# Kernel optimization log

Hardware: AMD Instinct MI355X
Metric: run time of the kernel (lower is better)

## Reference

```python
import jax, jax.numpy as jnp
import numpy as np

LMAX = 4
DSH = (LMAX + 1) ** 2          # 25 spherical-harmonic coefficients
C = 32                          # channels per degree l
N = 10000                       # nodes
E = 160000                      # edges
FC = 64                         # fc_len_in (radial/edge scalar feature dim)

# flattened (l,m) index = l^2 + l + m
IDX0 = np.array([l * l + l for l in range(LMAX + 1)])               # m = 0 coeffs
POS = {m: np.array([l * l + l + m for l in range(m, LMAX + 1)]) for m in range(1, LMAX + 1)}
NEG = {m: np.array([l * l + l - m for l in range(m, LMAX + 1)]) for m in range(1, LMAX + 1)}
L_OF_IDX = np.concatenate([np.full(2 * l + 1, l) for l in range(LMAX + 1)])  # degree of each coeff


def setup_inputs() -> dict:
    key = jax.random.key(0)
    ks = jax.random.split(key, 20)
    inp = {
        "x": jax.random.normal(ks[0], (N, DSH, C), jnp.float32),
        "wigner": jax.random.normal(ks[1], (E, DSH, DSH), jnp.float32) * 0.2,
        "edge_fc": jax.random.normal(ks[2], (E, FC), jnp.float32),
        "edge_src": jax.random.randint(ks[3], (E,), 0, N),
        "edge_dst": jax.random.randint(ks[4], (E,), 0, N),
    }
    # per-m SO(2) block weights
    d0 = (LMAX + 1) * C
    inp["w0"] = jax.random.normal(ks[5], (d0, d0), jnp.float32) / np.sqrt(d0)
    k = 6
    for m in range(1, LMAX + 1):
        dm = (LMAX + 1 - m) * C
        inp[f"w{m}r"] = jax.random.normal(ks[k], (dm, dm), jnp.float32) / np.sqrt(dm); k += 1
        inp[f"w{m}i"] = jax.random.normal(ks[k], (dm, dm), jnp.float32) / np.sqrt(dm); k += 1
    # radial/cfconv network producing per-(degree, channel) scales
    inp["fc_w"] = jax.random.normal(ks[k], (FC, (LMAX + 1) * C), jnp.float32) / np.sqrt(FC)
    inp["fc_b"] = jnp.zeros(((LMAX + 1) * C,), jnp.float32)
    return inp


def reference(x, wigner, edge_fc, edge_src, edge_dst,
              w0, w1r, w1i, w2r, w2i, w3r, w3i, w4r, w4i, fc_w, fc_b):
    Wr = {1: w1r, 2: w2r, 3: w3r, 4: w4r}
    Wi = {1: w1i, 2: w2i, 3: w3i, 4: w4i}
    # gather node features to edges and rotate into edge-aligned frame
    xe = x[edge_src]                                   # [E, 25, C]
    xr = jnp.einsum('eij,ejc->eic', wigner, xe)        # [E, 25, C]
    Ee = xr.shape[0]
    y = jnp.zeros_like(xr)
    # m = 0 block: real linear over stacked-l channels
    x0 = xr[:, IDX0, :].reshape(Ee, -1)                # [E, 5*C]
    y = y.at[:, IDX0, :].set((x0 @ w0).reshape(Ee, LMAX + 1, C))
    # m > 0 blocks: SO(2) complex-style mixing
    for m in range(1, LMAX + 1):
        pos, neg = POS[m], NEG[m]
        Lm = len(pos)
        xp = xr[:, pos, :].reshape(Ee, -1)             # [E, Lm*C]
        xn = xr[:, neg, :].reshape(Ee, -1)
        yp = xp @ Wr[m] - xn @ Wi[m]
        yn = xp @ Wi[m] + xn @ Wr[m]
        y = y.at[:, pos, :].set(yp.reshape(Ee, Lm, C))
        y = y.at[:, neg, :].set(yn.reshape(Ee, Lm, C))
    # cfconv: per-edge radial scaling, one scalar per (degree, channel)
    scale = jax.nn.silu(edge_fc @ fc_w + fc_b).reshape(Ee, LMAX + 1, C)
    y = y * scale[:, L_OF_IDX, :]
    # rotate back (Wigner D is orthogonal -> transpose is inverse)
    yb = jnp.einsum('eji,ejc->eic', wigner, y)
    # scatter-aggregate messages to destination nodes
    return jax.ops.segment_sum(yb, edge_dst, num_segments=N)
```

## Files before the change

kernel.cpp:

```cpp
#include <hip/hip_runtime.h>

typedef __attribute__((ext_vector_type(8))) short short8;
typedef __attribute__((ext_vector_type(4))) short short4v;
typedef __attribute__((ext_vector_type(4))) float f32x4;

#define MFMA16(a,b,c) __builtin_amdgcn_mfma_f32_16x16x32_bf16((a),(b),(c),0,0,0)

__device__ __align__(16) short g_wt[117760];
__device__ __align__(16) short g_wtf[148480];
__device__ __align__(16) short g_fcwt[10240];

struct K2Tab {
  int   fbase[50];
  int   pboff[50][8];
  short acoeff[50][8];
  short len[50];
  short dm[50];
  short ut[50];
  short ocoeff[50];
  short lsc[50];
  short co16[50];
  short pu[290];
  short pk[290];
};

constexpr K2Tab make_k2tab() {
  K2Tab T{};
  const int P[5][5]  = {{0,2,6,12,20},{3,7,13,21,0},{8,14,22,0,0},{15,23,0,0,0},{24,0,0,0,0}};
  const int Ng[5][5] = {{0,0,0,0,0},{1,5,11,19,0},{4,10,18,0,0},{9,17,0,0,0},{16,0,0,0,0}};
  const int WR[5]  = {0, 25600, 74752, 102400, 114688};
  const int WI[5]  = {0, 41984, 83968, 106496, 115712};
  const int NWI[5] = {0, 58368, 93184, 110592, 116736};
  const int ms[9]  = {1,1,2,2,0,3,3,4,4};
  const int hs[9]  = {0,1,0,1,0,0,1,0,1};
  const int ntc[9] = {8,8,6,6,10,4,4,2,2};
  int u = 0, fb = 0, np = 0;
  for (int g = 0; g < 9; ++g) {
    const int m = ms[g], h = hs[g];
    const int dm = (m == 0) ? 160 : (5 - m) * 32;
    const int lm = (m == 0) ? 5 : (5 - m);
    const int len = (m == 0) ? 5 : 2 * lm;
    const int b1 = (m == 0) ? 0 : ((h == 0) ? WR[m] : WI[m]);
    const int b2 = (m == 0) ? 0 : ((h == 0) ? NWI[m] : WR[m]);
    for (int tt = 0; tt < ntc[g]; ++tt, ++u) {
      T.dm[u] = (short)dm; T.len[u] = (short)len; T.ut[u] = (short)tt;
      const int lo = tt >> 1;
      T.ocoeff[u] = (short)((m == 0) ? P[0][lo] : ((h == 0) ? P[m][lo] : Ng[m][lo]));
      T.lsc[u] = (short)(m + lo);
      T.co16[u] = (short)((tt & 1) * 16);
      T.fbase[u] = fb;
      for (int k = 0; k < len; ++k) {
        int bb, ac;
        if (m == 0)      { bb = k * 32;            ac = P[0][k]; }
        else if (k < lm) { bb = b1 + k * 32;       ac = P[m][k]; }
        else             { bb = b2 + (k - lm) * 32; ac = Ng[m][k - lm]; }
        T.pboff[u][k] = bb; T.acoeff[u][k] = (short)ac;
        T.pu[np] = (short)u; T.pk[np] = (short)k; ++np;
      }
      fb += len * 512;
    }
  }
  return T;
}
__constant__ K2Tab c_kt = make_k2tab();

__device__ __forceinline__ short f2bf(float f) {
  unsigned u = __float_as_uint(f);
  u += 0x7FFFu + ((u >> 16) & 1u);
  return (short)(u >> 16);
}

__global__ void prep_weights(const float* __restrict__ w0,
    const float* __restrict__ w1r, const float* __restrict__ w1i,
    const float* __restrict__ w2r, const float* __restrict__ w2i,
    const float* __restrict__ w3r, const float* __restrict__ w3i,
    const float* __restrict__ w4r, const float* __restrict__ w4i,
    const float* __restrict__ fcw) {
  int idx = blockIdx.x * 256 + threadIdx.x;
  if (idx >= 128000) return;
  if (idx >= 117760) {
    int local = idx - 117760;
    int n = local >> 6, k = local & 63;
    g_fcwt[local] = f2bf(fcw[k * 160 + n]);
    return;
  }
  int off, dm; const float* src; bool neg = false;
  if (idx < 25600)       { off = 0;      dm = 160; src = w0;  }
  else if (idx < 41984)  { off = 25600;  dm = 128; src = w1r; }
  else if (idx < 58368)  { off = 41984;  dm = 128; src = w1i; }
  else if (idx < 74752)  { off = 58368;  dm = 128; src = w1i; neg = true; }
  else if (idx < 83968)  { off = 74752;  dm = 96;  src = w2r; }
  else if (idx < 93184)  { off = 83968;  dm = 96;  src = w2i; }
  else if (idx < 102400) { off = 93184;  dm = 96;  src = w2i; neg = true; }
  else if (idx < 106496) { off = 102400; dm = 64;  src = w3r; }
  else if (idx < 110592) { off = 106496; dm = 64;  src = w3i; }
  else if (idx < 114688) { off = 110592; dm = 64;  src = w3i; neg = true; }
  else if (idx < 115712) { off = 114688; dm = 32;  src = w4r; }
  else if (idx < 116736) { off = 115712; dm = 32;  src = w4i; }
  else                   { off = 116736; dm = 32;  src = w4i; neg = true; }
  int local = idx - off;
  int n = local / dm, k = local - n * dm;
  float v = src[k * dm + n];
  g_wt[idx] = f2bf(neg ? -v : v);
}

__global__ void prep_frags() {
  int i = blockIdx.x * 256 + threadIdx.x;
  if (i >= 290 * 512) return;
  int p = i >> 9;
  int w = i & 511;
  int lane = w >> 3, j = w & 7;
  int l15 = lane & 15, lg = lane >> 4;
  int u = c_kt.pu[p], k = c_kt.pk[p];
  int col = (int)c_kt.ut[u] * 16 + l15;
  g_wtf[i] = g_wt[c_kt.pboff[u][k] + col * (int)c_kt.dm[u] + lg * 8 + j];
}

__global__ void hist_kernel(const int* __restrict__ edst, int* __restrict__ cnt, int E) {
  int i = blockIdx.x * 256 + threadIdx.x;
  if (i < E) atomicAdd(&cnt[edst[i]], 1);
}

__global__ __launch_bounds__(1024) void scan_kernel(
    const int* __restrict__ cnt, int* __restrict__ cursor, int N) {
  __shared__ int s[1024];
  const int t = threadIdx.x;
  int v[10]; int sum = 0;
  #pragma unroll
  for (int k = 0; k < 10; ++k) {
    int i = t * 10 + k;
    v[k] = (i < N) ? cnt[i] : 0;
    sum += v[k];
  }
  s[t] = sum;
  __syncthreads();
  for (int d = 1; d < 1024; d <<= 1) {
    int add = (t >= d) ? s[t - d] : 0;
    __syncthreads();
    s[t] += add;
    __syncthreads();
  }
  int prefix = s[t] - sum;
  #pragma unroll
  for (int k = 0; k < 10; ++k) {
    int i = t * 10 + k;
    if (i < N) cursor[i] = prefix;
    prefix += v[k];
  }
}

__global__ void scatter_kernel(const int* __restrict__ edst, int* __restrict__ cursor,
                               int* __restrict__ order, int E) {
  int i = blockIdx.x * 256 + threadIdx.x;
  if (i < E) {
    int p = atomicAdd(&cursor[edst[i]], 1);
    order[p] = i;
  }
}

#define ESTRIDE 1048
#define SMEM_K12 78080

__global__ __launch_bounds__(512, 4) void k12_fused(
    const float* __restrict__ x, const float* __restrict__ wig,
    const float* __restrict__ efc, const int* __restrict__ esrc,
    const int* __restrict__ order, const float* __restrict__ fcb,
    short* __restrict__ y, int E)
{
  extern __shared__ char smem[];
  short*     s_buf  = (short*)smem;
  _Float16*  s_sc   = (_Float16*)(smem + 67072);
  int*       s_meta = (int*)(smem + 77824);

  const int tid = threadIdx.x;
  const int lane = tid & 63;
  const int wid = tid >> 6;
  const int l15 = lane & 15;
  const int lg  = lane >> 4;
  const int koff = lg * 8;
  const int e0  = blockIdx.x * 32;

  for (int o = tid; o < 3584; o += 512) {
    int e = o / 112, q = o - e * 112;
    ((int*)s_buf)[e * 524 + 400 + q] = 0;
  }
  if (tid < 32) {
    int idx = min(e0 + tid, E - 1);
    int og = order[idx];
    s_meta[tid] = og;
    s_meta[32 + tid] = esrc[og];
  }
  __syncthreads();

  for (int o = tid; o < 25600; o += 512) {
    int e = o / 800, q = o - e * 800;
    s_buf[e * ESTRIDE + q] = f2bf(x[(size_t)s_meta[32 + e] * 800 + q]);
  }
  {
    const int mt = wid >> 2;
    const int ge = s_meta[mt * 16 + l15];
    const float* ep = efc + (size_t)ge * 64;
    float4 fa = *(const float4*)(ep + lg * 8);
    float4 fb = *(const float4*)(ep + lg * 8 + 4);
    float4 fc = *(const float4*)(ep + 32 + lg * 8);
    float4 fd = *(const float4*)(ep + 32 + lg * 8 + 4);
    short8 af0, af1;
    af0[0]=f2bf(fa.x); af0[1]=f2bf(fa.y); af0[2]=f2bf(fa.z); af0[3]=f2bf(fa.w);
    af0[4]=f2bf(fb.x); af0[5]=f2bf(fb.y); af0[6]=f2bf(fb.z); af0[7]=f2bf(fb.w);
    af1[0]=f2bf(fc.x); af1[1]=f2bf(fc.y); af1[2]=f2bf(fc.z); af1[3]=f2bf(fc.w);
    af1[4]=f2bf(fd.x); af1[5]=f2bf(fd.y); af1[6]=f2bf(fd.z); af1[7]=f2bf(fd.w);
    for (int nt = (wid & 3); nt < 10; nt += 4) {
      const int f = nt * 16 + l15;
      const short* bp = g_fcwt + f * 64 + lg * 8;
      short8 b0 = *(const short8*)(bp);
      short8 b1 = *(const short8*)(bp + 32);
      f32x4 acc = {0.f, 0.f, 0.f, 0.f};
      acc = MFMA16(af0, b0, acc);
      acc = MFMA16(af1, b1, acc);
      float bias = fcb[f];
      #pragma unroll
      for (int r = 0; r < 4; ++r) {
        float vv = acc[r] + bias;
        s_sc[(mt * 16 + lg * 4 + r) * 168 + (f >> 5) * 33 + (f & 31)] =
            (_Float16)(vv / (1.f + __expf(-vv)));
      }
    }
  }
  __syncthreads();

  #pragma unroll 4
  for (int i = 0; i < 4; ++i) {
    const int e = wid * 4 + i;
    short* eb = s_buf + e * ESTRIDE;
    const float* wp = wig + (size_t)s_meta[e] * 625;
    short8 a0, a1;
    #pragma unroll
    for (int j = 0; j < 8; ++j) {
      const int k = koff + j;
      a0[j] = eb[k * 32 + l15];
      a1[j] = eb[k * 32 + 16 + l15];
    }
    short8 b0, b1;
    const int r1 = min(16 + l15, 24);
    #pragma unroll
    for (int j = 0; j < 8; ++j) {
      const int k = koff + j;
      const int kc = min(k, 24);
      const short v0 = f2bf(wp[l15 * 25 + kc]);
      const short v1 = f2bf(wp[r1 * 25 + kc]);
      b0[j] = (k < 25) ? v0 : (short)0;
      b1[j] = (k < 25) ? v1 : (short)0;
    }
    f32x4 d00 = {0.f,0.f,0.f,0.f}, d01 = {0.f,0.f,0.f,0.f};
    f32x4 d10 = {0.f,0.f,0.f,0.f}, d11 = {0.f,0.f,0.f,0.f};
    d00 = MFMA16(a0, b0, d00);
    d01 = MFMA16(a0, b1, d01);
    d10 = MFMA16(a1, b0, d10);
    d11 = MFMA16(a1, b1, d11);
    short4v v;
    v[0]=f2bf(d00[0]); v[1]=f2bf(d00[1]); v[2]=f2bf(d00[2]); v[3]=f2bf(d00[3]);
    *(short4v*)(eb + l15 * 32 + lg * 4) = v;
    v[0]=f2bf(d10[0]); v[1]=f2bf(d10[1]); v[2]=f2bf(d10[2]); v[3]=f2bf(d10[3]);
    *(short4v*)(eb + l15 * 32 + 16 + lg * 4) = v;
    if (l15 < 9) {
      v[0]=f2bf(d01[0]); v[1]=f2bf(d01[1]); v[2]=f2bf(d01[2]); v[3]=f2bf(d01[3]);
      *(short4v*)(eb + (16 + l15) * 32 + lg * 4) = v;
      v[0]=f2bf(d11[0]); v[1]=f2bf(d11[1]); v[2]=f2bf(d11[2]); v[3]=f2bf(d11[3]);
      *(short4v*)(eb + (16 + l15) * 32 + 16 + lg * 4) = v;
    }
  }
  __syncthreads();

  for (int u = wid; u < 50; u += 8) {
    const int len = c_kt.len[u];
    const short* Bp = g_wtf + c_kt.fbase[u] + lane * 8;
    short8 B[8];
    #pragma unroll 8
    for (int k = 0; k < 8; ++k)
      if (k < len) B[k] = *(const short8*)(Bp + (k << 9));
    const int co = c_kt.co16[u] + l15;
    const int oc = c_kt.ocoeff[u];
    const int ls = c_kt.lsc[u];
    #pragma unroll 2
    for (int mt = 0; mt < 2; ++mt) {
      const short* xl = s_buf + (mt * 16 + l15) * ESTRIDE + koff;
      f32x4 acc0 = {0.f,0.f,0.f,0.f}, acc1 = {0.f,0.f,0.f,0.f};
      #pragma unroll 8
      for (int k = 0; k < 8; ++k) {
        if (k < len) {
          short8 a = *(const short8*)(xl + (int)c_kt.acoeff[u][k] * 32);
          if (k & 1) acc1 = MFMA16(a, B[k], acc1);
          else       acc0 = MFMA16(a, B[k], acc0);
        }
      }
      f32x4 acc = acc0 + acc1;
      #pragma unroll
      for (int r = 0; r < 4; ++r) {
        const int el = mt * 16 + lg * 4 + r;
        const int slot = e0 + el;
        if (slot < E) {
          float sc = (float)s_sc[el * 168 + ls * 33 + co];
          y[(size_t)slot * 800 + oc * 32 + co] = f2bf(acc[r] * sc);
        }
      }
    }
  }
}

__global__ __launch_bounds__(256, 5) void k3_back(
    const short* __restrict__ y, const float* __restrict__ wig,
    const int* __restrict__ edst, const int* __restrict__ order,
    const int* __restrict__ cnt, float* __restrict__ out, int E)
{
  __shared__ __align__(16) char sumem[27136];
  __shared__ int s_meta[64];
  short* s_y  = (short*)sumem;
  float* yb_s = (float*)sumem;

  const int tid = threadIdx.x;
  const int lane = tid & 63;
  const int wid = tid >> 6;
  const int l15 = lane & 15;
  const int lg  = lane >> 4;
  const int e0  = blockIdx.x * 8;

  for (int o = tid; o < 5216; o += 256) ((int*)sumem)[o] = 0;
  if (tid < 8) {
    int idx = e0 + tid;
    bool v = idx < E;
    int og = order[v ? idx : 0];
    s_meta[tid] = og;
    s_meta[16 + tid] = v ? edst[og] : -1;
  }
  __syncthreads();

  if (wid == 0) {
    int dj = (lane < 8) ? s_meta[16 + lane] : -1;
    bool valid = (lane < 8) && (dj >= 0);
    bool is_start = valid && (lane == 0 || dj != s_meta[16 + lane - 1]);
    unsigned long long vm = __ballot(valid);
    unsigned long long sm = __ballot(is_start);
    int nv = __popcll(vm);
    int ng = __popcll(sm);
    if (lane == 0) s_meta[24] = ng;
    if ((int)lane < ng) {
      int s = -1, c = -1;
      for (int b = 0; b < 8; ++b) { if ((sm >> b) & 1) { ++c; if (c == (int)lane) { s = b; break; } } }
      int e_ = nv;
      for (int b = s + 1; b < 8; ++b) if ((sm >> b) & 1) { e_ = b; break; }
      int d = s_meta[16 + s];
      s_meta[25 + lane] = d;
      s_meta[33 + lane] = s;
      s_meta[41 + lane] = e_;
      s_meta[49 + lane] = ((e_ - s) == cnt[d]) ? 1 : 0;
    }
  }
  for (int o = tid; o < 800; o += 256) {
    int e = o / 100, r = o - e * 100;
    int slot = min(e0 + e, E - 1);
    int q = r * 8;
    *(short8*)(s_y + e * 1304 + (q >> 5) * 40 + (q & 31)) =
        *(const short8*)(y + (size_t)slot * 800 + q);
  }
  __syncthreads();

  f32x4 r00[2], r01[2], r10[2], r11[2];
  #pragma unroll
  for (int i = 0; i < 2; ++i) {
    const int e = wid * 2 + i;
    const short* yb = s_y + e * 1304 + lg * 8 * 40;
    const float* wp = wig + (size_t)s_meta[e] * 625;
    short8 a0, a1, b0, b1;
    const int c2 = min(16 + l15, 24);
    #pragma unroll 8
    for (int j = 0; j < 8; ++j) {
      a0[j] = yb[j * 40 + l15];
      a1[j] = yb[j * 40 + 16 + l15];
      const int k = lg * 8 + j;
      const int kc = min(k, 24);
      const short v0 = f2bf(wp[kc * 25 + l15]);
      const short v1 = f2bf(wp[kc * 25 + c2]);
      b0[j] = (k < 25) ? v0 : (short)0;
      b1[j] = (k < 25) ? v1 : (short)0;
    }
    f32x4 d00 = {0.f,0.f,0.f,0.f}, d01 = {0.f,0.f,0.f,0.f};
    f32x4 d10 = {0.f,0.f,0.f,0.f}, d11 = {0.f,0.f,0.f,0.f};
    d00 = MFMA16(a0, b0, d00);
    d01 = MFMA16(a0, b1, d01);
    d10 = MFMA16(a1, b0, d10);
    d11 = MFMA16(a1, b1, d11);
    r00[i] = d00; r01[i] = d01; r10[i] = d10; r11[i] = d11;
  }
  __syncthreads();

  #pragma unroll
  for (int i = 0; i < 2; ++i) {
    const int e = wid * 2 + i;
    float* yb = yb_s + e * 840;
    #pragma unroll 4
    for (int r = 0; r < 4; ++r) {
      yb[l15 * 33 + lg * 4 + r]      = r00[i][r];
      yb[l15 * 33 + 16 + lg * 4 + r] = r10[i][r];
    }
    if (l15 < 9) {
      #pragma unroll 4
      for (int r = 0; r < 4; ++r) {
        yb[(16 + l15) * 33 + lg * 4 + r]      = r01[i][r];
        yb[(16 + l15) * 33 + 16 + lg * 4 + r] = r11[i][r];
      }
    }
  }
  __syncthreads();

  const int ng = s_meta[24];
  for (int o = tid; o < 800; o += 256) {
    const int yoff = (o >> 5) * 33 + (o & 31);
    for (int g = 0; g < ng; ++g) {
      float sum = 0.f;
      const int gs = s_meta[33 + g], ge = s_meta[41 + g];
      for (int e = gs; e < ge; ++e) sum += yb_s[e * 840 + yoff];
      float* ad = out + (size_t)s_meta[25 + g] * 800 + o;
      if (s_meta[49 + g]) *ad = sum;
      else atomicAdd(ad, sum);
    }
  }
}

extern "C" void kernel_launch(void* const* d_in, const int* in_sizes, int n_in,
                              void* d_out, int out_size, void* d_ws, size_t ws_size,
                              hipStream_t stream) {
  const float* x    = (const float*)d_in[0];
  const float* wigp = (const float*)d_in[1];
  const float* efc  = (const float*)d_in[2];
  const int*   esrc = (const int*)d_in[3];
  const int*   edst = (const int*)d_in[4];
  const float* w0   = (const float*)d_in[5];
  const float* w1r  = (const float*)d_in[6];
  const float* w1i  = (const float*)d_in[7];
  const float* w2r  = (const float*)d_in[8];
  const float* w2i  = (const float*)d_in[9];
  const float* w3r  = (const float*)d_in[10];
  const float* w3i  = (const float*)d_in[11];
  const float* w4r  = (const float*)d_in[12];
  const float* w4i  = (const float*)d_in[13];
  const float* fcw  = (const float*)d_in[14];
  const float* fcb  = (const float*)d_in[15];
  float* out = (float*)d_out;
  const int E = in_sizes[3];
  const int N = out_size / 800;

  int* cnt    = (int*)d_ws;
  int* cursor = cnt + N;
  int* order  = cnt + 2 * N;
  size_t y_off = (((size_t)(2 * N + E) * 4) + 255) & ~(size_t)255;
  short* yb = (short*)((char*)d_ws + y_off);

  hipFuncSetAttribute((const void*)k12_fused,
                      hipFuncAttributeMaxDynamicSharedMemorySize, SMEM_K12);

  prep_weights<<<(128000 + 255) / 256, 256, 0, stream>>>(
      w0, w1r, w1i, w2r, w2i, w3r, w3i, w4r, w4i, fcw);
  prep_frags<<<(290 * 512 + 255) / 256, 256, 0, stream>>>();

  hipMemsetAsync(d_out, 0, (size_t)out_size * sizeof(float), stream);
  hipMemsetAsync(cnt, 0, (size_t)N * sizeof(int), stream);

  hist_kernel<<<(E + 255) / 256, 256, 0, stream>>>(edst, cnt, E);
  scan_kernel<<<1, 1024, 0, stream>>>(cnt, cursor, N);
  scatter_kernel<<<(E + 255) / 256, 256, 0, stream>>>(edst, cursor, order, E);

  k12_fused<<<(E + 31) / 32, 512, SMEM_K12, stream>>>(
      x, wigp, efc, esrc, order, fcb, yb, E);
  k3_back<<<(E + 7) / 8, 256, 0, stream>>>(yb, wigp, edst, order, cnt, out, E);
}
```

Baseline: 770.3 us.

## Fuse forward rotation, SO(2) mixing, back-rotation and scatter into one kernel

Merges k12_fused and k3_back into a single kernel handling 16 edges per block, so the intermediate message y stays in shared memory instead of being written to global memory in bf16 and read back. The destination-segment grouping moves into the fused kernel, and the per-block edge count is halved so the shared-memory footprint fits. This removes a global round-trip and one kernel launch. In exchange, per-block work drops, weight fragments are reloaded for every 16 edges, and segment reduction groups are smaller, which may mean more atomics.

```diff
diff --git a/kernel.cpp b/kernel.cpp
--- a/kernel.cpp
+++ b/kernel.cpp
@@ -159,18 +159,22 @@
 }
 
 #define ESTRIDE 1048
-#define SMEM_K12 78080
-
-__global__ __launch_bounds__(512, 4) void k12_fused(
+#define YSTRIDE 1024
+#define SMEM_ALL 72144
+
+__global__ __launch_bounds__(512, 4) void k_all(
     const float* __restrict__ x, const float* __restrict__ wig,
     const float* __restrict__ efc, const int* __restrict__ esrc,
-    const int* __restrict__ order, const float* __restrict__ fcb,
-    short* __restrict__ y, int E)
+    const int* __restrict__ edst, const int* __restrict__ order,
+    const float* __restrict__ fcb, const int* __restrict__ cnt,
+    float* __restrict__ out, int E)
 {
   extern __shared__ char smem[];
-  short*     s_buf  = (short*)smem;
-  _Float16*  s_sc   = (_Float16*)(smem + 67072);
-  int*       s_meta = (int*)(smem + 77824);
+  short*    s_buf  = (short*)smem;
+  short*    s_y    = (short*)(smem + 33536);
+  _Float16* s_sc   = (_Float16*)(smem + 66304);
+  int*      s_meta = (int*)(smem + 71680);
+  float*    yb_s   = (float*)smem;
 
   const int tid = threadIdx.x;
   const int lane = tid & 63;
@@ -178,27 +182,54 @@
   const int l15 = lane & 15;
   const int lg  = lane >> 4;
   const int koff = lg * 8;
-  const int e0  = blockIdx.x * 32;
-
-  for (int o = tid; o < 3584; o += 512) {
+  const int e0  = blockIdx.x * 16;
+
+  for (int o = tid; o < 1792; o += 512) {
     int e = o / 112, q = o - e * 112;
     ((int*)s_buf)[e * 524 + 400 + q] = 0;
   }
-  if (tid < 32) {
-    int idx = min(e0 + tid, E - 1);
-    int og = order[idx];
+  for (int o = tid; o < 1792; o += 512) {
+    int e = o / 112, q = o - e * 112;
+    ((int*)s_y)[e * 512 + 400 + q] = 0;
+  }
+  if (tid < 16) {
+    int idx = e0 + tid;
+    bool v = idx < E;
+    int og = order[v ? idx : 0];
     s_meta[tid] = og;
-    s_meta[32 + tid] = esrc[og];
-  }
-  __syncthreads();
-
-  for (int o = tid; o < 25600; o += 512) {
+    s_meta[16 + tid] = esrc[og];
+    s_meta[32 + tid] = v ? edst[og] : -1;
+  }
+  __syncthreads();
+
+  if (wid == 0) {
+    int dj = (lane < 16) ? s_meta[32 + lane] : -1;
+    bool valid = (lane < 16) && (dj >= 0);
+    bool is_start = valid && (lane == 0 || dj != s_meta[32 + lane - 1]);
+    unsigned long long vm = __ballot(valid);
+    unsigned long long sm = __ballot(is_start);
+    int nv = __popcll(vm);
+    int ng = __popcll(sm);
+    if (lane == 0) s_meta[48] = ng;
+    if ((int)lane < ng) {
+      int s = -1, c = -1;
+      for (int b = 0; b < 16; ++b) { if ((sm >> b) & 1) { ++c; if (c == (int)lane) { s = b; break; } } }
+      int e_ = nv;
+      for (int b = s + 1; b < 16; ++b) if ((sm >> b) & 1) { e_ = b; break; }
+      int d = s_meta[32 + s];
+      s_meta[49 + lane] = d;
+      s_meta[65 + lane] = s;
+      s_meta[81 + lane] = e_;
+      s_meta[97 + lane] = ((e_ - s) == cnt[d]) ? 1 : 0;
+    }
+  }
+
+  for (int o = tid; o < 12800; o += 512) {
     int e = o / 800, q = o - e * 800;
-    s_buf[e * ESTRIDE + q] = f2bf(x[(size_t)s_meta[32 + e] * 800 + q]);
+    s_buf[e * ESTRIDE + q] = f2bf(x[(size_t)s_meta[16 + e] * 800 + q]);
   }
   {
-    const int mt = wid >> 2;
-    const int ge = s_meta[mt * 16 + l15];
+    const int ge = s_meta[l15];
     const float* ep = efc + (size_t)ge * 64;
     float4 fa = *(const float4*)(ep + lg * 8);
     float4 fb = *(const float4*)(ep + lg * 8 + 4);
@@ -209,7 +240,7 @@
     af0[4]=f2bf(fb.x); af0[5]=f2bf(fb.y); af0[6]=f2bf(fb.z); af0[7]=f2bf(fb.w);
     af1[0]=f2bf(fc.x); af1[1]=f2bf(fc.y); af1[2]=f2bf(fc.z); af1[3]=f2bf(fc.w);
     af1[4]=f2bf(fd.x); af1[5]=f2bf(fd.y); af1[6]=f2bf(fd.z); af1[7]=f2bf(fd.w);
-    for (int nt = (wid & 3); nt < 10; nt += 4) {
+    for (int nt = wid; nt < 10; nt += 8) {
       const int f = nt * 16 + l15;
       const short* bp = g_fcwt + f * 64 + lg * 8;
       short8 b0 = *(const short8*)(bp);
@@ -221,16 +252,16 @@
       #pragma unroll
       for (int r = 0; r < 4; ++r) {
         float vv = acc[r] + bias;
-        s_sc[(mt * 16 + lg * 4 + r) * 168 + (f >> 5) * 33 + (f & 31)] =
+        s_sc[(lg * 4 + r) * 168 + (f >> 5) * 33 + (f & 31)] =
             (_Float16)(vv / (1.f + __expf(-vv)));
       }
     }
   }
   __syncthreads();
 
-  #pragma unroll 4
-  for (int i = 0; i < 4; ++i) {
-    const int e = wid * 4 + i;
+  #pragma unroll 2
+  for (int i = 0; i < 2; ++i) {
+    const int e = wid * 2 + i;
     short* eb = s_buf + e * ESTRIDE;
     const float* wp = wig + (size_t)s_meta[e] * 625;
     short8 a0, a1;
@@ -281,102 +312,39 @@
     const int co = c_kt.co16[u] + l15;
     const int oc = c_kt.ocoeff[u];
     const int ls = c_kt.lsc[u];
-    #pragma unroll 2
-    for (int mt = 0; mt < 2; ++mt) {
-      const short* xl = s_buf + (mt * 16 + l15) * ESTRIDE + koff;
-      f32x4 acc0 = {0.f,0.f,0.f,0.f}, acc1 = {0.f,0.f,0.f,0.f};
-      #pragma unroll 8
-      for (int k = 0; k < 8; ++k) {
-        if (k < len) {
-          short8 a = *(const short8*)(xl + (int)c_kt.acoeff[u][k] * 32);
-          if (k & 1) acc1 = MFMA16(a, B[k], acc1);
-          else       acc0 = MFMA16(a, B[k], acc0);
-        }
+    const short* xl = s_buf + l15 * ESTRIDE + koff;
+    f32x4 acc0 = {0.f,0.f,0.f,0.f}, acc1 = {0.f,0.f,0.f,0.f};
+    #pragma unroll 8
+    for (int k = 0; k < 8; ++k) {
+      if (k < len) {
+        short8 a = *(const short8*)(xl + (int)c_kt.acoeff[u][k] * 32);
+        if (k & 1) acc1 = MFMA16(a, B[k], acc1);
+        else       acc0 = MFMA16(a, B[k], acc0);
       }
-      f32x4 acc = acc0 + acc1;
-      #pragma unroll
-      for (int r = 0; r < 4; ++r) {
-        const int el = mt * 16 + lg * 4 + r;
-        const int slot = e0 + el;
-        if (slot < E) {
-          float sc = (float)s_sc[el * 168 + ls * 33 + co];
-          y[(size_t)slot * 800 + oc * 32 + co] = f2bf(acc[r] * sc);
-        }
-      }
-    }
-  }
-}
-
-__global__ __launch_bounds__(256, 5) void k3_back(
-    const short* __restrict__ y, const float* __restrict__ wig,
-    const int* __restrict__ edst, const int* __restrict__ order,
-    const int* __restrict__ cnt, float* __restrict__ out, int E)
-{
-  __shared__ __align__(16) char sumem[27136];
-  __shared__ int s_meta[64];
-  short* s_y  = (short*)sumem;
-  float* yb_s = (float*)sumem;
-
-  const int tid = threadIdx.x;
-  const int lane = tid & 63;
-  const int wid = tid >> 6;
-  const int l15 = lane & 15;
-  const int lg  = lane >> 4;
-  const int e0  = blockIdx.x * 8;
-
-  for (int o = tid; o < 5216; o += 256) ((int*)sumem)[o] = 0;
-  if (tid < 8) {
-    int idx = e0 + tid;
-    bool v = idx < E;
-    int og = order[v ? idx : 0];
-    s_meta[tid] = og;
-    s_meta[16 + tid] = v ? edst[og] : -1;
-  }
-  __syncthreads();
-
-  if (wid == 0) {
-    int dj = (lane < 8) ? s_meta[16 + lane] : -1;
-    bool valid = (lane < 8) && (dj >= 0);
-    bool is_start = valid && (lane == 0 || dj != s_meta[16 + lane - 1]);
-    unsigned long long vm = __ballot(valid);
-    unsigned long long sm = __ballot(is_start);
-    int nv = __popcll(vm);
-    int ng = __popcll(sm);
-    if (lane == 0) s_meta[24] = ng;
-    if ((int)lane < ng) {
-      int s = -1, c = -1;
-      for (int b = 0; b < 8; ++b) { if ((sm >> b) & 1) { ++c; if (c == (int)lane) { s = b; break; } } }
-      int e_ = nv;
-      for (int b = s + 1; b < 8; ++b) if ((sm >> b) & 1) { e_ = b; break; }
-      int d = s_meta[16 + s];
-      s_meta[25 + lane] = d;
-      s_meta[33 + lane] = s;
-      s_meta[41 + lane] = e_;
-      s_meta[49 + lane] = ((e_ - s) == cnt[d]) ? 1 : 0;
-    }
-  }
-  for (int o = tid; o < 800; o += 256) {
-    int e = o / 100, r = o - e * 100;
-    int slot = min(e0 + e, E - 1);
-    int q = r * 8;
-    *(short8*)(s_y + e * 1304 + (q >> 5) * 40 + (q & 31)) =
-        *(const short8*)(y + (size_t)slot * 800 + q);
+    }
+    f32x4 acc = acc0 + acc1;
+    #pragma unroll
+    for (int r = 0; r < 4; ++r) {
+      const int el = lg * 4 + r;
+      float sc = (float)s_sc[el * 168 + ls * 33 + co];
+      s_y[el * YSTRIDE + oc * 32 + co] = f2bf(acc[r] * sc);
+    }
   }
   __syncthreads();
 
   f32x4 r00[2], r01[2], r10[2], r11[2];
-  #pragma unroll
+  #pragma unroll 2
   for (int i = 0; i < 2; ++i) {
     const int e = wid * 2 + i;
-    const short* yb = s_y + e * 1304 + lg * 8 * 40;
+    const short* yb = s_y + e * YSTRIDE;
     const float* wp = wig + (size_t)s_meta[e] * 625;
     short8 a0, a1, b0, b1;
     const int c2 = min(16 + l15, 24);
     #pragma unroll 8
     for (int j = 0; j < 8; ++j) {
-      a0[j] = yb[j * 40 + l15];
-      a1[j] = yb[j * 40 + 16 + l15];
-      const int k = lg * 8 + j;
+      const int k = koff + j;
+      a0[j] = yb[k * 32 + l15];
+      a1[j] = yb[k * 32 + 16 + l15];
       const int kc = min(k, 24);
       const short v0 = f2bf(wp[kc * 25 + l15]);
       const short v1 = f2bf(wp[kc * 25 + c2]);
@@ -393,7 +361,7 @@
   }
   __syncthreads();
 
-  #pragma unroll
+  #pragma unroll 2
   for (int i = 0; i < 2; ++i) {
     const int e = wid * 2 + i;
     float* yb = yb_s + e * 840;
@@ -412,15 +380,15 @@
   }
   __syncthreads();
 
-  const int ng = s_meta[24];
-  for (int o = tid; o < 800; o += 256) {
+  const int ng = s_meta[48];
+  for (int o = tid; o < 800; o += 512) {
     const int yoff = (o >> 5) * 33 + (o & 31);
     for (int g = 0; g < ng; ++g) {
       float sum = 0.f;
-      const int gs = s_meta[33 + g], ge = s_meta[41 + g];
+      const int gs = s_meta[65 + g], ge = s_meta[81 + g];
       for (int e = gs; e < ge; ++e) sum += yb_s[e * 840 + yoff];
-      float* ad = out + (size_t)s_meta[25 + g] * 800 + o;
-      if (s_meta[49 + g]) *ad = sum;
+      float* ad = out + (size_t)s_meta[49 + g] * 800 + o;
+      if (s_meta[97 + g]) *ad = sum;
       else atomicAdd(ad, sum);
     }
   }
@@ -452,11 +420,9 @@
   int* cnt    = (int*)d_ws;
   int* cursor = cnt + N;
   int* order  = cnt + 2 * N;
-  size_t y_off = (((size_t)(2 * N + E) * 4) + 255) & ~(size_t)255;
-  short* yb = (short*)((char*)d_ws + y_off);
-
-  hipFuncSetAttribute((const void*)k12_fused,
-                      hipFuncAttributeMaxDynamicSharedMemorySize, SMEM_K12);
+
+  hipFuncSetAttribute((const void*)k_all,
+                      hipFuncAttributeMaxDynamicSharedMemorySize, SMEM_ALL);
 
   prep_weights<<<(128000 + 255) / 256, 256, 0, stream>>>(
       w0, w1r, w1i, w2r, w2i, w3r, w3i, w4r, w4i, fcw);
@@ -469,7 +435,6 @@
   scan_kernel<<<1, 1024, 0, stream>>>(cnt, cursor, N);
   scatter_kernel<<<(E + 255) / 256, 256, 0, stream>>>(edst, cursor, order, E);
 
-  k12_fused<<<(E + 31) / 32, 512, SMEM_K12, stream>>>(
-      x, wigp, efc, esrc, order, fcb, yb, E);
-  k3_back<<<(E + 7) / 8, 256, 0, stream>>>(yb, wigp, edst, order, cnt, out, E);
-}
+  k_all<<<(E + 15) / 16, 512, SMEM_ALL, stream>>>(
+      x, wigp, efc, esrc, edst, order, fcb, cnt, out, E);
+}
```

After: 704.2 us. 1.09x faster.
